# Kernel tuning notes

Hardware: AMD Instinct MI355X
Metric: run time of the kernel (lower is better)

## Reference

```python
import math
import jax, jax.numpy as jnp
import numpy as np

EPS = 1e-5  # BatchNorm2d default eps


def setup_inputs() -> dict:
    key = jax.random.key(0)
    ks = jax.random.split(key, 12)
    C, I = 256, 128  # in_channels, inter_channels (= C // reduction)
    n, h, w = 4, 64, 64
    s = 0.02
    return {
        "x": jax.random.normal(ks[0], (n, C, h, w), jnp.float32),
        "g_w": jax.random.normal(ks[1], (I, C), jnp.float32) * s,
        "g_b": jax.random.normal(ks[2], (I,), jnp.float32) * s,
        "theta_w": jax.random.normal(ks[3], (I, C), jnp.float32) * s,
        "theta_b": jax.random.normal(ks[4], (I,), jnp.float32) * s,
        "phi_w": jax.random.normal(ks[5], (I, C), jnp.float32) * s,
        "phi_b": jax.random.normal(ks[6], (I,), jnp.float32) * s,
        "out_w": jax.random.normal(ks[7], (C, I), jnp.float32) * s,
        "bn_gamma": jax.random.uniform(ks[8], (C,), jnp.float32, 0.5, 1.5),
        "bn_beta": jax.random.normal(ks[9], (C,), jnp.float32) * s,
        "bn_mean": jax.random.normal(ks[10], (C,), jnp.float32) * s,
        "bn_var": jax.random.uniform(ks[11], (C,), jnp.float32, 0.5, 1.5),
    }


def reference(x, g_w, g_b, theta_w, theta_b, phi_w, phi_b, out_w,
              bn_gamma, bn_beta, bn_mean, bn_var):
    n, c, h, w = x.shape
    xf = x.reshape(n, c, h * w)  # (n, C, N)

    def proj(Wm, b):  # 1x1 conv == per-position linear: (n, I, N)
        return jnp.einsum('ic,ncp->nip', Wm, xf) + b[None, :, None]

    g_x = proj(g_w, g_b)          # (n, I, N)
    theta_x = proj(theta_w, theta_b)  # (n, I, N)
    phi_x = proj(phi_w, phi_b)        # (n, I, N)

    # dot_product mode: softmax FIRST, then divide by sqrt(C) (faithful to source)
    scores = jnp.einsum('nip,niq->npq', theta_x, phi_x)  # (n, N, N)
    attn = jax.nn.softmax(scores, axis=-1) / math.sqrt(c)

    y = jnp.einsum('npq,niq->nip', attn, g_x)  # (n, I, N)
    y = y.reshape(n, -1, h, w)                 # (n, I, h, w)

    # conv_out: 1x1 conv (no bias) + BatchNorm2d (eval-mode running stats)
    y = jnp.einsum('oi,nihw->nohw', out_w, y)  # (n, C, h, w)
    inv = bn_gamma / jnp.sqrt(bn_var + EPS)
    y = y * inv[None, :, None, None] + (bn_beta - bn_mean * inv)[None, :, None, None]
    return y + x
```

## Files before the change

### kernel.cpp

```cpp
#include <hip/hip_runtime.h>

typedef short short8 __attribute__((ext_vector_type(8)));
typedef short short4v __attribute__((ext_vector_type(4)));
typedef float f32x4 __attribute__((ext_vector_type(4)));
typedef float f32x16 __attribute__((ext_vector_type(16)));
typedef unsigned int uint4v __attribute__((ext_vector_type(4)));
typedef unsigned int uint2v __attribute__((ext_vector_type(2)));

#define NB 4
#define CD 256
#define ID 128
#define NP 4096

static __device__ __forceinline__ short f2bf(float f){
  unsigned u = __float_as_uint(f);
  u += 0x7FFF + ((u >> 16) & 1);
  return (short)(u >> 16);
}
static __device__ __forceinline__ float bf2f(short s){
  unsigned u = ((unsigned)(unsigned short)s) << 16;
  return __uint_as_float(u);
}
static __device__ __forceinline__ unsigned cvtpk(float lo, float hi){
  unsigned r;
  asm("v_cvt_pk_bf16_f32 %0, %1, %2" : "=v"(r) : "v"(lo), "v"(hi));
  return r;
}
static __device__ __forceinline__ float fexp2(float x){
  float r;
  asm("v_exp_f32 %0, %1" : "=v"(r) : "v"(x));
  return r;
}
static __device__ __forceinline__ unsigned pack4_fp8(float a, float b, float c, float d){
  unsigned lo, hi;
  asm("v_cvt_pk_fp8_f32 %0, %1, %2" : "=v"(lo) : "v"(a), "v"(b));
  asm("v_cvt_pk_fp8_f32 %0, %1, %2" : "=v"(hi) : "v"(c), "v"(d));
  return (lo & 0xffffu) | (hi << 16);
}
static __device__ __forceinline__ unsigned char f2fp8(float v){
  unsigned u;
  asm("v_cvt_pk_fp8_f32 %0, %1, %1" : "=v"(u) : "v"(v));
  return (unsigned char)u;
}

static __device__ __forceinline__ void gload16(const void* g, void* l){
  __builtin_amdgcn_global_load_lds(
      (const __attribute__((address_space(1))) unsigned int*)g,
      (__attribute__((address_space(3))) unsigned int*)l, 16, 0, 0);
}

__global__ __launch_bounds__(256) void k_cvtw(const float* __restrict__ g_w,
    const float* __restrict__ th_w, const float* __restrict__ ph_w,
    const float* __restrict__ out_w, short* __restrict__ wb){
  int idx = (blockIdx.x * 256 + threadIdx.x) * 4;
  const float* s;
  int sel = idx >> 15;
  if(sel == 0) s = g_w; else if(sel == 1) s = th_w; else if(sel == 2) s = ph_w; else s = out_w;
  int off = idx & 32767;
  float4 v = *reinterpret_cast<const float4*>(s + off);
  short4v o = { f2bf(v.x), f2bf(v.y), f2bf(v.z), f2bf(v.w) };
  *reinterpret_cast<short4v*>(wb + idx) = o;
}

__global__ __launch_bounds__(256) void k_transpose(const float* __restrict__ x,
                                                   short* __restrict__ xt){
  __shared__ float T[64][68];
  int n = blockIdx.z, c0 = blockIdx.y * 64, p0 = blockIdx.x * 64;
  int t = threadIdx.x;
  const float* xp = x + ((size_t)(n * CD + c0)) * NP + p0;
#pragma unroll
  for(int it = 0; it < 4; ++it){
    int c = (t >> 4) + it * 16;
    int p = (t & 15) * 4;
    float4 v = *reinterpret_cast<const float4*>(xp + (size_t)c * NP + p);
    T[c][p+0] = v.x; T[c][p+1] = v.y; T[c][p+2] = v.z; T[c][p+3] = v.w;
  }
  __syncthreads();
  short* op = xt + ((size_t)(n * NP + p0)) * CD + c0;
  int p = t >> 2, cc = (t & 3) * 16;
  short8 a, b;
#pragma unroll
  for(int j = 0; j < 8; ++j){ a[j] = f2bf(T[cc + j][p]); b[j] = f2bf(T[cc + 8 + j][p]); }
  *reinterpret_cast<short8*>(op + (size_t)p * CD + cc) = a;
  *reinterpret_cast<short8*>(op + (size_t)p * CD + cc + 8) = b;
}

__global__ __launch_bounds__(512) void k_proj(const short* __restrict__ xt,
    const short* __restrict__ wb, const float* __restrict__ g_b,
    const float* __restrict__ th_b, const float* __restrict__ ph_b,
    unsigned char* __restrict__ q8, unsigned char* __restrict__ k8,
    unsigned char* __restrict__ v8){
  __shared__ __align__(16) char XT[32768];
  int b = blockIdx.x;
  int n = b >> 6, pt = b & 63;
  int pb0 = pt * 64;
  int t = threadIdx.x, w = t >> 6, l = t & 63;
  int lr = l & 15, lg = l >> 4;
  int i0 = w * 16;

  const char* xg = (const char*)(xt + ((size_t)(n * NP + pb0)) * CD);
#pragma unroll
  for(int i_ = 0; i_ < 4; ++i_){
    int dd = t * 16 + i_ * 8192;
    int row = dd >> 9;
    int sz = (dd & ~511) | ((dd & 511) ^ ((row & 15) << 4));
    gload16(xg + sz, XT + dd);
  }

  const short* gww = wb;
  const short* thw = wb + 32768;
  const short* phw = wb + 65536;
  short8 Wt[8], Wp[8], Wg[8];
#pragma unroll
  for(int kk = 0; kk < 8; ++kk){
    size_t wo = (size_t)(i0 + lr) * CD + kk * 32 + lg * 8;
    Wt[kk] = *reinterpret_cast<const short8*>(thw + wo);
    Wp[kk] = *reinterpret_cast<const short8*>(phw + wo);
    Wg[kk] = *reinterpret_cast<const short8*>(gww + wo);
  }
  float bt = th_b[i0 + lr];
  float bp = ph_b[i0 + lr];
  float gb[4];
#pragma unroll
  for(int r = 0; r < 4; ++r) gb[r] = g_b[i0 + lg * 4 + r];

  __syncthreads();

  size_t pan = ((size_t)n * 64 + pt) * 64;
#pragma unroll
  for(int psub = 0; psub < 4; ++psub){
    int prow = psub * 16 + lr;
    short8 X[8];
#pragma unroll
    for(int kk = 0; kk < 8; ++kk)
      X[kk] = *reinterpret_cast<const short8*>(
          XT + prow * 512 + ((kk * 64 + lg * 16) ^ ((prow & 15) << 4)));
    f32x4 aT = {0.f,0.f,0.f,0.f}, aP = {0.f,0.f,0.f,0.f}, aG = {0.f,0.f,0.f,0.f};
#pragma unroll
    for(int kk = 0; kk < 8; ++kk){
      aT = __builtin_amdgcn_mfma_f32_16x16x32_bf16(X[kk], Wt[kk], aT, 0, 0, 0);
      aP = __builtin_amdgcn_mfma_f32_16x16x32_bf16(X[kk], Wp[kk], aP, 0, 0, 0);
      aG = __builtin_amdgcn_mfma_f32_16x16x32_bf16(Wg[kk], X[kk], aG, 0, 0, 0);
    }
#pragma unroll
    for(int r = 0; r < 4; ++r){
      size_t o = ((size_t)(n * NP + pb0 + psub * 16 + lg * 4 + r)) * ID + i0 + lr;
      q8[o] = f2fp8((aT[r] + bt) * 1.44269504f);
      k8[o] = f2fp8(aP[r] + bp);
    }
#pragma unroll
    for(int r = 0; r < 4; ++r){
      int ii = i0 + lg * 4 + r;
      v8[(pan + (ii >> 1)) * 128 + (ii & 1) * 64 + psub * 16 + lr] = f2fp8(aG[r] + gb[r]);
    }
  }
}

__global__ __launch_bounds__(256, 2) void k_attn(const unsigned char* __restrict__ q8,
    const unsigned char* __restrict__ k8, const unsigned char* __restrict__ v8,
    short* __restrict__ po, float* __restrict__ psums){
  __shared__ __align__(16) char smem[65536];
  int b = blockIdx.x;
  int xcd = b & 7;
  int n = xcd >> 1;
  int kq = ((xcd & 1) << 1) | ((b >> 3) & 1);
  int qtl = b >> 4;
  int t = threadIdx.x, w = t >> 6, l = t & 63;
  int q31 = l & 31, hi = l >> 5;
  int pbase = qtl * 128 + w * 32;

  const char* kpanel = (const char*)k8 + ((size_t)(n * NP + kq * 1024)) * ID;
  const char* vpanel = (const char*)v8 + ((size_t)n * 64 + kq * 16) * 8192;
  const char* qbase  = (const char*)q8 + ((size_t)(n * NP + pbase)) * ID;

  uint2v Qf[8];
#pragma unroll
  for(int cst = 0; cst < 8; ++cst)
    Qf[cst] = *reinterpret_cast<const uint2v*>(qbase + q31 * 128 + cst * 16 + hi * 8);

  f32x16 Of[4];
#pragma unroll
  for(int db = 0; db < 4; ++db)
#pragma unroll
    for(int r = 0; r < 16; ++r) Of[db][r] = 0.f;
  float ps = 0.f;

#define STAGE(cb, kt_) do { \
    const char* kg_ = kpanel + (size_t)(kt_) * 8192; \
    const char* vg_ = vpanel + (size_t)(kt_) * 8192; \
    char* kld_ = smem + (cb) * 8192; \
    char* vld_ = smem + 16384 + (cb) * 8192; \
    _Pragma("unroll") \
    for(int i_ = 0; i_ < 2; ++i_){ \
      int dd = t * 16 + i_ * 4096; \
      int sz = (dd & ~127) | ((dd & 127) ^ (((dd >> 7) & 7) << 4)); \
      gload16(kg_ + sz, kld_ + dd); \
      gload16(vg_ + sz, vld_ + dd); \
    } \
  } while(0)

  STAGE(0, 0);
  __syncthreads();

#pragma unroll 2
  for(int kt = 0; kt < 16; ++kt){
    const int pb = kt & 1;
    if(kt + 1 < 16) STAGE(pb ^ 1, kt + 1);
    const char* Kc = smem + pb * 8192;
    const char* Vc = smem + 16384 + pb * 8192;
#pragma unroll
    for(int kb = 0; kb < 2; ++kb){
      f32x16 S;
#pragma unroll
      for(int r = 0; r < 16; ++r) S[r] = 0.f;
      int krow = kb * 32 + q31;
      __builtin_amdgcn_s_setprio(1);
#pragma unroll
      for(int cst = 0; cst < 8; ++cst){
        uint2v Kf = *reinterpret_cast<const uint2v*>(
            Kc + krow * 128 + ((cst * 16) ^ ((krow & 7) << 4)) + hi * 8);
        S = __builtin_amdgcn_mfma_f32_32x32x16_fp8_fp8(
            __builtin_bit_cast(long, Kf), __builtin_bit_cast(long, Qf[cst]), S, 0, 0, 0);
      }
      __builtin_amdgcn_s_setprio(0);
      float e[16];
#pragma unroll
      for(int r = 0; r < 16; ++r) e[r] = fexp2(S[r] - 4.0f);
#pragma unroll
      for(int r = 0; r < 16; ++r) ps += e[r];
      unsigned u0 = pack4_fp8(e[0],  e[1],  e[2],  e[3]);
      unsigned u1 = pack4_fp8(e[4],  e[5],  e[6],  e[7]);
      unsigned u2 = pack4_fp8(e[8],  e[9],  e[10], e[11]);
      unsigned u3 = pack4_fp8(e[12], e[13], e[14], e[15]);
      asm("v_permlane32_swap_b32 %0, %1" : "+v"(u0), "+v"(u1));
      asm("v_permlane32_swap_b32 %0, %1" : "+v"(u2), "+v"(u3));
      __builtin_amdgcn_s_setprio(1);
#pragma unroll
      for(int cc = 0; cc < 2; ++cc){
        uint2v Pa = cc ? uint2v{u2, u3} : uint2v{u0, u1};
        long Pl = __builtin_bit_cast(long, Pa);
#pragma unroll
        for(int db = 0; db < 4; ++db){
          int d = db * 32 + q31;
          int row = d >> 1;
          int off = (d & 1) * 64 + kb * 32 + cc * 16;
          uint2v Vf = *reinterpret_cast<const uint2v*>(
              Vc + row * 128 + ((off ^ ((row & 7) << 4))) + hi * 8);
          Of[db] = __builtin_amdgcn_mfma_f32_32x32x16_fp8_fp8(
              Pl, __builtin_bit_cast(long, Vf), Of[db], 0, 0, 0);
        }
      }
      __builtin_amdgcn_s_setprio(0);
    }
    __syncthreads();
  }
#undef STAGE

  float pst = ps + __shfl_xor(ps, 32);
  if(hi == 0)
    psums[(size_t)kq * 16384 + n * NP + pbase + q31] = pst;

  float* ow = (float*)(smem + w * 16384);
#pragma unroll
  for(int reg = 0; reg < 16; ++reg){
    int q = (reg & 3) + 8 * (reg >> 2) + 4 * hi;
#pragma unroll
    for(int db = 0; db < 4; ++db)
      ow[q * 128 + db * 32 + q31] = Of[db][reg];
  }
  asm volatile("s_waitcnt lgkmcnt(0)" ::: "memory");
  __builtin_amdgcn_sched_barrier(0);
  short* pr = po + ((size_t)kq * 16384 + n * NP + pbase) * ID;
#pragma unroll
  for(int it = 0; it < 8; ++it){
    int o = it * 1024 + l * 16;
    int q = o >> 8, d0 = (o & 255) >> 1;
    f32x4 va = *reinterpret_cast<const f32x4*>(ow + q * 128 + d0);
    f32x4 vb = *reinterpret_cast<const f32x4*>(ow + q * 128 + d0 + 4);
    uint4v pk4 = { cvtpk(va[0], va[1]), cvtpk(va[2], va[3]),
                   cvtpk(vb[0], vb[1]), cvtpk(vb[2], vb[3]) };
    *reinterpret_cast<short8*>(pr + (size_t)q * ID + d0) = __builtin_bit_cast(short8, pk4);
  }
}

__global__ __launch_bounds__(512) void k_outproj(const short* __restrict__ po,
    const float* __restrict__ psums, const short* __restrict__ ow_b,
    const float* __restrict__ bng, const float* __restrict__ bnb,
    const float* __restrict__ bnm, const float* __restrict__ bnv,
    const float* __restrict__ x, float* __restrict__ out){
  __shared__ __align__(16) short XW[64 * 128];
  int b = blockIdx.x;
  int n = b >> 6, pt = b & 63;
  int pg0 = pt * 64;
  int t = threadIdx.x, w = t >> 6, l = t & 63;
  int lr = l & 15, lg = l >> 4;

  {
    int p = t >> 3, i0 = (t & 7) * 16;
    size_t qg = (size_t)n * NP + pg0 + p;
    float den = psums[qg] + psums[16384 + qg] + psums[32768 + qg] + psums[49152 + qg];
    float inv = 1.f / (16.f * den);
    const short* pp = po + qg * ID + i0;
    int key = (p & 15) << 4;
#pragma unroll
    for(int h = 0; h < 2; ++h){
      short8 b0 = *reinterpret_cast<const short8*>(pp + h * 8);
      short8 b1 = *reinterpret_cast<const short8*>(pp + (size_t)16384 * ID + h * 8);
      short8 b2 = *reinterpret_cast<const short8*>(pp + (size_t)32768 * ID + h * 8);
      short8 b3 = *reinterpret_cast<const short8*>(pp + (size_t)49152 * ID + h * 8);
      float f[8];
#pragma unroll
      for(int j = 0; j < 8; ++j)
        f[j] = (bf2f(b0[j]) + bf2f(b1[j]) + bf2f(b2[j]) + bf2f(b3[j])) * inv;
      uint4v pkv = { cvtpk(f[0], f[1]), cvtpk(f[2], f[3]),
                     cvtpk(f[4], f[5]), cvtpk(f[6], f[7]) };
      *reinterpret_cast<short8*>((char*)XW + p * 256 + ((i0 * 2 + h * 16) ^ key)) =
          __builtin_bit_cast(short8, pkv);
    }
  }
  __syncthreads();

  int c0 = w * 32;
  f32x4 acc[2][4];
#pragma unroll
  for(int mf = 0; mf < 2; ++mf)
#pragma unroll
    for(int nf = 0; nf < 4; ++nf) acc[mf][nf] = {0.f,0.f,0.f,0.f};
#pragma unroll
  for(int kk = 0; kk < 4; ++kk){
    short8 Af[2];
#pragma unroll
    for(int mf = 0; mf < 2; ++mf)
      Af[mf] = *reinterpret_cast<const short8*>(ow_b + (size_t)(c0 + mf * 16 + lr) * ID + kk * 32 + lg * 8);
#pragma unroll
    for(int nf = 0; nf < 4; ++nf){
      int prow = nf * 16 + lr;
      short8 Bf = *reinterpret_cast<const short8*>(
          (char*)XW + prow * 256 + ((kk * 64 + lg * 16) ^ ((prow & 15) << 4)));
#pragma unroll
      for(int mf = 0; mf < 2; ++mf)
        acc[mf][nf] = __builtin_amdgcn_mfma_f32_16x16x32_bf16(Af[mf], Bf, acc[mf][nf], 0, 0, 0);
    }
  }

#pragma unroll
  for(int mf = 0; mf < 2; ++mf){
    int cb = c0 + mf * 16 + lg * 4;
    float inv[4], sh[4];
#pragma unroll
    for(int r = 0; r < 4; ++r){
      float iv = bng[cb + r] * rsqrtf(bnv[cb + r] + 1e-5f);
      inv[r] = iv;
      sh[r] = bnb[cb + r] - bnm[cb + r] * iv;
    }
#pragma unroll
    for(int nf = 0; nf < 4; ++nf){
      int p = pg0 + nf * 16 + lr;
#pragma unroll
      for(int r = 0; r < 4; ++r){
        size_t idx = ((size_t)(n * CD + cb + r)) * NP + p;
        out[idx] = acc[mf][nf][r] * inv[r] + sh[r] + x[idx];
      }
    }
  }
}

extern "C" void kernel_launch(void* const* d_in, const int* in_sizes, int n_in,
                              void* d_out, int out_size, void* d_ws, size_t ws_size,
                              hipStream_t stream){
  const float* x    = (const float*)d_in[0];
  const float* g_w  = (const float*)d_in[1];
  const float* g_b  = (const float*)d_in[2];
  const float* th_w = (const float*)d_in[3];
  const float* th_b = (const float*)d_in[4];
  const float* ph_w = (const float*)d_in[5];
  const float* ph_b = (const float*)d_in[6];
  const float* out_w= (const float*)d_in[7];
  const float* bng  = (const float*)d_in[8];
  const float* bnb  = (const float*)d_in[9];
  const float* bnm  = (const float*)d_in[10];
  const float* bnv  = (const float*)d_in[11];
  float* out = (float*)d_out;
  char* ws = (char*)d_ws;

  short* xt          = (short*)(ws);
  unsigned char* q8  = (unsigned char*)(ws + (size_t)(8u  << 20));
  unsigned char* k8  = (unsigned char*)(ws + (size_t)(12u << 20));
  unsigned char* v8  = (unsigned char*)(ws + (size_t)(16u << 20));
  short* wb          = (short*)(ws + (size_t)(24u << 20));
  short* po          = (short*)(ws + (size_t)(25u << 20));
  float* psum        = (float*)(ws + (size_t)(41u << 20));

  k_cvtw<<<128, 256, 0, stream>>>(g_w, th_w, ph_w, out_w, wb);
  k_transpose<<<dim3(64, 4, 4), 256, 0, stream>>>(x, xt);
  k_proj<<<256, 512, 0, stream>>>(xt, wb, g_b, th_b, ph_b, q8, k8, v8);
  k_attn<<<512, 256, 0, stream>>>(q8, k8, v8, po, psum);
  k_outproj<<<256, 512, 0, stream>>>(po, psum, wb + 98304, bng, bnb, bnm, bnv, x, out);
}
```

Baseline: 67.95 us.

## Relayout K and V in global memory for 128-bit LDS fragment reads

The projection kernel now writes K with a permuted channel order and V in a blocked layout. In the attention kernel each lane can then fetch two MFMA operand fragments with one 16-byte LDS read instead of two 8-byte swizzled reads. V staging becomes a straight copy and K staging uses a new address map. The aim is to halve LDS read instructions and drop the XOR swizzle arithmetic, at the risk of LDS bank conflicts from the unswizzled row-stride-16 pattern and less coalesced global writes in the producer.

```diff
diff --git a/kernel.cpp b/kernel.cpp
--- a/kernel.cpp
+++ b/kernel.cpp
@@ -120,13 +120,15 @@
   }
   float bt = th_b[i0 + lr];
   float bp = ph_b[i0 + lr];
+  int ik = i0 + lr;
+  int ip = (ik & 7) | (((ik >> 4) & 1) << 3) | (((ik >> 3) & 1) << 4) | ((ik >> 5) << 5);
   float gb[4];
 #pragma unroll
   for(int r = 0; r < 4; ++r) gb[r] = g_b[i0 + lg * 4 + r];
 
   __syncthreads();
 
-  size_t pan = ((size_t)n * 64 + pt) * 64;
+  size_t vbase = ((size_t)n * 64 + pt) * 8192;
 #pragma unroll
   for(int psub = 0; psub < 4; ++psub){
     int prow = psub * 16 + lr;
@@ -144,14 +146,15 @@
     }
 #pragma unroll
     for(int r = 0; r < 4; ++r){
-      size_t o = ((size_t)(n * NP + pb0 + psub * 16 + lg * 4 + r)) * ID + i0 + lr;
-      q8[o] = f2fp8((aT[r] + bt) * 1.44269504f);
-      k8[o] = f2fp8(aP[r] + bp);
+      size_t row = (size_t)(n * NP + pb0 + psub * 16 + lg * 4 + r);
+      q8[row * ID + i0 + lr] = f2fp8((aT[r] + bt) * 1.44269504f);
+      k8[row * ID + ip]      = f2fp8(aP[r] + bp);
     }
 #pragma unroll
     for(int r = 0; r < 4; ++r){
       int ii = i0 + lg * 4 + r;
-      v8[(pan + (ii >> 1)) * 128 + (ii & 1) * 64 + psub * 16 + lr] = f2fp8(aG[r] + gb[r]);
+      v8[vbase + (psub >> 1) * 4096 + ((lr >> 3) & 1) * 2048 + ii * 16
+               + (psub & 1) * 8 + (lr & 7)] = f2fp8(aG[r] + gb[r]);
     }
   }
 }
@@ -193,9 +196,9 @@
     _Pragma("unroll") \
     for(int i_ = 0; i_ < 2; ++i_){ \
       int dd = t * 16 + i_ * 4096; \
-      int sz = (dd & ~127) | ((dd & 127) ^ (((dd >> 7) & 7) << 4)); \
-      gload16(kg_ + sz, kld_ + dd); \
-      gload16(vg_ + sz, vld_ + dd); \
+      int ks = (((dd >> 4) & 63) << 7) | ((dd >> 11) << 5) | (((dd >> 10) & 1) << 4); \
+      gload16(kg_ + ks, kld_ + dd); \
+      gload16(vg_ + dd, vld_ + dd); \
     } \
   } while(0)
 
@@ -216,11 +219,15 @@
       int krow = kb * 32 + q31;
       __builtin_amdgcn_s_setprio(1);
 #pragma unroll
-      for(int cst = 0; cst < 8; ++cst){
-        uint2v Kf = *reinterpret_cast<const uint2v*>(
-            Kc + krow * 128 + ((cst * 16) ^ ((krow & 7) << 4)) + hi * 8);
+      for(int cp = 0; cp < 4; ++cp){
+        uint4v Kp = *reinterpret_cast<const uint4v*>(
+            Kc + cp * 2048 + hi * 1024 + krow * 16);
+        uint2v Ka = { Kp[0], Kp[1] };
+        uint2v Kb2 = { Kp[2], Kp[3] };
         S = __builtin_amdgcn_mfma_f32_32x32x16_fp8_fp8(
-            __builtin_bit_cast(long, Kf), __builtin_bit_cast(long, Qf[cst]), S, 0, 0, 0);
+            __builtin_bit_cast(long, Ka), __builtin_bit_cast(long, Qf[2*cp]), S, 0, 0, 0);
+        S = __builtin_amdgcn_mfma_f32_32x32x16_fp8_fp8(
+            __builtin_bit_cast(long, Kb2), __builtin_bit_cast(long, Qf[2*cp+1]), S, 0, 0, 0);
       }
       __builtin_amdgcn_s_setprio(0);
       float e[16];
@@ -234,21 +241,20 @@
       unsigned u3 = pack4_fp8(e[12], e[13], e[14], e[15]);
       asm("v_permlane32_swap_b32 %0, %1" : "+v"(u0), "+v"(u1));
       asm("v_permlane32_swap_b32 %0, %1" : "+v"(u2), "+v"(u3));
+      long P0 = __builtin_bit_cast(long, uint2v{u0, u1});
+      long P1 = __builtin_bit_cast(long, uint2v{u2, u3});
       __builtin_amdgcn_s_setprio(1);
 #pragma unroll
-      for(int cc = 0; cc < 2; ++cc){
-        uint2v Pa = cc ? uint2v{u2, u3} : uint2v{u0, u1};
-        long Pl = __builtin_bit_cast(long, Pa);
-#pragma unroll
-        for(int db = 0; db < 4; ++db){
-          int d = db * 32 + q31;
-          int row = d >> 1;
-          int off = (d & 1) * 64 + kb * 32 + cc * 16;
-          uint2v Vf = *reinterpret_cast<const uint2v*>(
-              Vc + row * 128 + ((off ^ ((row & 7) << 4))) + hi * 8);
-          Of[db] = __builtin_amdgcn_mfma_f32_32x32x16_fp8_fp8(
-              Pl, __builtin_bit_cast(long, Vf), Of[db], 0, 0, 0);
-        }
+      for(int db = 0; db < 4; ++db){
+        int d = db * 32 + q31;
+        uint4v Vp = *reinterpret_cast<const uint4v*>(
+            Vc + kb * 4096 + hi * 2048 + d * 16);
+        uint2v Va = { Vp[0], Vp[1] };
+        uint2v Vb = { Vp[2], Vp[3] };
+        Of[db] = __builtin_amdgcn_mfma_f32_32x32x16_fp8_fp8(
+            P0, __builtin_bit_cast(long, Va), Of[db], 0, 0, 0);
+        Of[db] = __builtin_amdgcn_mfma_f32_32x32x16_fp8_fp8(
+            P1, __builtin_bit_cast(long, Vb), Of[db], 0, 0, 0);
       }
       __builtin_amdgcn_s_setprio(0);
     }
```

New measurement: 66.49 us. 2.1% less time.
